# Kernel optimization log

Measured on AMD Instinct MI355X. Metric: run time of the kernel, lower is better.

The kernel has to match this reference:

```python
import jax, jax.numpy as jnp
import numpy as np

H1, H, OUT, T = 512, 2048, 1024, 4096

def setup_inputs() -> dict:
    key = jax.random.key(0)
    ks = jax.random.split(key, 20)
    s = 0.02
    return {
        "input": jax.random.normal(ks[0], (1, OUT), jnp.float32),
        "hidden": jax.random.normal(ks[1], (1, 1, H), jnp.float32) * 0.1,
        "encoder_outputs": jax.random.normal(ks[2], (T, H), jnp.float32),
        "prenet_w": jax.random.normal(ks[3], (H1, OUT), jnp.float32) * s,
        "prenet_b": jnp.zeros((H1,), jnp.float32),
        "prenet2_w": jax.random.normal(ks[4], (H, H1), jnp.float32) * s,
        "prenet2_b": jnp.zeros((H,), jnp.float32),
        "attn1_w": jax.random.normal(ks[5], (H, H), jnp.float32) * s,
        "attn2_w": jax.random.normal(ks[6], (H, H), jnp.float32) * s,
        "attn3_w": jax.random.normal(ks[7], (1, H), jnp.float32) * s,
        "gru_w_ih": jax.random.normal(ks[8], (3 * H, 2 * H), jnp.float32) * s,
        "gru_w_hh": jax.random.normal(ks[9], (3 * H, H), jnp.float32) * s,
        "gru_b_ih": jnp.zeros((3 * H,), jnp.float32),
        "gru_b_hh": jnp.zeros((3 * H,), jnp.float32),
        "lin_w": jax.random.normal(ks[10], (OUT, H), jnp.float32) * s,
        "lin_b": jnp.zeros((OUT,), jnp.float32),
    }

def reference(input, hidden, encoder_outputs, prenet_w, prenet_b, prenet2_w,
              prenet2_b, attn1_w, attn2_w, attn3_w, gru_w_ih, gru_w_hh,
              gru_b_ih, gru_b_hh, lin_w, lin_b):
    # prenet MLP (dropout in eval mode = identity)
    em6 = jax.nn.relu(jax.nn.relu(input @ prenet_w.T + prenet_b) @ prenet2_w.T + prenet2_b)  # [1,H]
    # Bahdanau additive attention
    way = em6 @ attn1_w.T                                 # [1,H]
    uah = encoder_outputs @ attn2_w.T                     # [T,H]
    beta = jnp.tanh(way + uah)                            # [T,H] (broadcast = expand_as)
    gamma = beta @ attn3_w.T                              # [T,1]
    attn_weights = jax.nn.softmax(gamma.T, axis=1)        # [1,T]
    attn_applied = attn_weights @ encoder_outputs         # [1,H]
    # single-step GRU (PyTorch gate order: r, z, n)
    x = jnp.concatenate([em6, attn_applied], axis=1)      # [1,2H]
    h0 = hidden[0]                                        # [1,H]
    gi = x @ gru_w_ih.T + gru_b_ih                        # [1,3H]
    gh = h0 @ gru_w_hh.T + gru_b_hh                       # [1,3H]
    i_r, i_z, i_n = jnp.split(gi, 3, axis=1)
    h_r, h_z, h_n = jnp.split(gh, 3, axis=1)
    r = jax.nn.sigmoid(i_r + h_r)
    z = jax.nn.sigmoid(i_z + h_z)
    n = jnp.tanh(i_n + r * h_n)
    h_new = (1.0 - z) * n + z * h0                        # [1,H]
    out = jax.nn.softmax(h_new @ lin_w.T + lin_b, axis=1) # [1,OUT]
    return out, h_new[None], attn_weights
```

## Files before the change

kernel.cpp:

```cpp
#include <hip/hip_runtime.h>
#include <hip/hip_bf16.h>

typedef __bf16 bf16x8 __attribute__((ext_vector_type(8)));
typedef __bf16 bf16x4 __attribute__((ext_vector_type(4)));
typedef float f32x4 __attribute__((ext_vector_type(4)));

#define H1 512
#define H 2048
#define OUTN 1024
#define T 4096

__global__ __launch_bounds__(256) void matvec_k(
    const float* __restrict__ W, const float* __restrict__ x,
    const float* __restrict__ b, float* __restrict__ out,
    int R, int K, int relu)
{
    int row = blockIdx.x * 4 + (threadIdx.x >> 6);
    int lane = threadIdx.x & 63;
    if (row >= R) return;
    const float* Wr = W + (size_t)row * K;
    float s = 0.f;
    for (int k = lane * 4; k < K; k += 256) {
        float4 w4 = *(const float4*)(Wr + k);
        float4 x4 = *(const float4*)(x + k);
        s += w4.x * x4.x + w4.y * x4.y + w4.z * x4.z + w4.w * x4.w;
    }
    #pragma unroll
    for (int m = 32; m; m >>= 1) s += __shfl_xor(s, m, 64);
    if (lane == 0) {
        if (b) s += b[row];
        if (relu) s = fmaxf(s, 0.f);
        out[row] = s;
    }
}

__global__ __launch_bounds__(256) void cvt_frag_k(
    const float* __restrict__ E, const float* __restrict__ W2,
    __bf16* __restrict__ dst)
{
    const int EC = T * H / 8;
    int c = blockIdx.x * 256 + threadIdx.x;
    const float* src;
    __bf16* d;
    if (c < EC) {
        int lane = c & 63;
        int k32 = (c >> 6) & 63;
        int r16 = c >> 12;
        int row = r16 * 16 + (lane & 15);
        int col = k32 * 32 + (lane >> 4) * 8;
        src = E + (size_t)row * H + col;
        d = dst + (size_t)c * 8;
    } else {
        int c2 = c - EC;
        int row = c2 >> 8;
        int kc = c2 & 255;
        src = W2 + (size_t)row * H + kc * 8;
        int grp = kc >> 3, cc = kc & 7;
        int sw = cc ^ (row & 7);
        d = dst + (size_t)T * H + (size_t)row * H + grp * 64 + sw * 8;
    }
    float4 a = *(const float4*)src;
    float4 b = *(const float4*)(src + 4);
    bf16x8 v = {(__bf16)a.x, (__bf16)a.y, (__bf16)a.z, (__bf16)a.w,
                (__bf16)b.x, (__bf16)b.y, (__bf16)b.z, (__bf16)b.w};
    *(bf16x8*)d = v;
}

__global__ __launch_bounds__(256, 4) void gamma_gemm8(
    const __bf16* __restrict__ Efrag,
    const __bf16* __restrict__ Bsw,
    const float* __restrict__ way, const float* __restrict__ a3,
    float* __restrict__ gamma)
{
    __shared__ __attribute__((aligned(16))) __bf16 Bs[64][64];
    __shared__ float wayS[64], a3S[64];

    const int tb = blockIdx.x, hb = blockIdx.y;
    const int tid = threadIdx.x, lane = tid & 63, wid = tid >> 6;
    if (tid < 64) { wayS[tid] = way[hb * 64 + tid]; a3S[tid] = a3[hb * 64 + tid]; }

    const int K = 2048;
    const int rl = lane & 15;
    const int kg = (lane >> 4) * 8;
    const __bf16* Abase = Efrag + (((size_t)(tb * 8 + wid * 2) * 64) * 64 + lane) * 8;
    const __bf16* Bp = Bsw + (size_t)(hb * 64) * K;

    f32x4 acc[2][4] = {};

    for (int t = 0; t < 32; ++t) {
        const int k0 = t * 64;
        #pragma unroll
        for (int j = 0; j < 2; ++j) {
            int c = tid + j * 256;
            int row_ = c >> 3, cc_ = c & 7;
            const __bf16* s_ = Bp + (size_t)row_ * K + k0 + cc_ * 8;
            __builtin_amdgcn_global_load_lds(
                (const __attribute__((address_space(1))) void*)s_,
                (__attribute__((address_space(3))) void*)((char*)&Bs[0][0] + c * 16),
                16, 0, 0);
        }
        bf16x8 af[2][2];
        #pragma unroll
        for (int mi = 0; mi < 2; ++mi)
            #pragma unroll
            for (int kk = 0; kk < 2; ++kk)
                af[mi][kk] = *(const bf16x8*)(Abase +
                    ((size_t)(mi * 64 + t * 2 + kk) * 64) * 8);

        __syncthreads();

        #pragma unroll
        for (int kk = 0; kk < 2; ++kk) {
            bf16x8 bfm[4];
            const int kb = (kg + kk * 32) * 2;
            #pragma unroll
            for (int ni = 0; ni < 4; ++ni) {
                int r_ = ni * 16 + rl;
                bfm[ni] = *(const bf16x8*)((const char*)&Bs[0][0] + r_ * 128 + (kb ^ ((r_ & 7) << 4)));
            }
            #pragma unroll
            for (int mi = 0; mi < 2; ++mi)
                #pragma unroll
                for (int ni = 0; ni < 4; ++ni)
                    acc[mi][ni] = __builtin_amdgcn_mfma_f32_16x16x32_bf16(
                        af[mi][kk], bfm[ni], acc[mi][ni], 0, 0, 0);
        }
        __syncthreads();
    }

    const int rg = lane >> 4;
    #pragma unroll
    for (int mi = 0; mi < 2; ++mi) {
        float sr[4] = {0.f, 0.f, 0.f, 0.f};
        #pragma unroll
        for (int ni = 0; ni < 4; ++ni) {
            int h = ni * 16 + rl;
            float wh = wayS[h];
            float ah = a3S[h];
            #pragma unroll
            for (int r = 0; r < 4; ++r)
                sr[r] += tanhf(wh + acc[mi][ni][r]) * ah;
        }
        #pragma unroll
        for (int m = 1; m < 16; m <<= 1) {
            #pragma unroll
            for (int r = 0; r < 4; ++r)
                sr[r] += __shfl_xor(sr[r], m, 64);
        }
        if (rl == 0) {
            int t = tb * 128 + wid * 32 + mi * 16 + rg * 4;
            #pragma unroll
            for (int r = 0; r < 4; ++r)
                atomicAdd(&gamma[t + r], sr[r]);
        }
    }
}

#define BM 128
#define BN 128
#define BK 32
#define LSTR 40

__global__ __launch_bounds__(256) void gamma_gemm(
    const float* __restrict__ E, const float* __restrict__ W2,
    const float* __restrict__ way, const float* __restrict__ a3,
    float* __restrict__ gamma)
{
    __shared__ __bf16 As[BM][LSTR];
    __shared__ __bf16 Bs[BN][LSTR];
    __shared__ float wayS[BN];
    __shared__ float a3S[BN];

    const int tb = blockIdx.x, hb = blockIdx.y;
    const int tid = threadIdx.x, lane = tid & 63, wid = tid >> 6;
    const int wr = wid >> 1, wc = wid & 1;
    if (tid < BN) { wayS[tid] = way[hb * BN + tid]; a3S[tid] = a3[hb * BN + tid]; }

    f32x4 acc[4][4] = {};
    const int K = 2048;
    const float* Ep  = E  + (size_t)(tb * BM) * K;
    const float* W2p = W2 + (size_t)(hb * BN) * K;
    const int rl = lane & 15;
    const int kg = (lane >> 4) * 8;

    for (int k0 = 0; k0 < K; k0 += BK) {
        __syncthreads();
        #pragma unroll
        for (int i = 0; i < 4; ++i) {
            int c = tid + i * 256;
            int row = c >> 3;
            int col = (c & 7) * 4;
            float4 va = *(const float4*)(Ep + (size_t)row * K + k0 + col);
            bf16x4 pa = {(__bf16)va.x, (__bf16)va.y, (__bf16)va.z, (__bf16)va.w};
            *(bf16x4*)&As[row][col] = pa;
            float4 vb = *(const float4*)(W2p + (size_t)row * K + k0 + col);
            bf16x4 pb = {(__bf16)vb.x, (__bf16)vb.y, (__bf16)vb.z, (__bf16)vb.w};
            *(bf16x4*)&Bs[row][col] = pb;
        }
        __syncthreads();
        bf16x8 af[4], bfr[4];
        #pragma unroll
        for (int mi = 0; mi < 4; ++mi)
            af[mi] = *(const bf16x8*)&As[wr * 64 + mi * 16 + rl][kg];
        #pragma unroll
        for (int ni = 0; ni < 4; ++ni)
            bfr[ni] = *(const bf16x8*)&Bs[wc * 64 + ni * 16 + rl][kg];
        #pragma unroll
        for (int mi = 0; mi < 4; ++mi)
            #pragma unroll
            for (int ni = 0; ni < 4; ++ni)
                acc[mi][ni] = __builtin_amdgcn_mfma_f32_16x16x32_bf16(
                    af[mi], bfr[ni], acc[mi][ni], 0, 0, 0);
    }

    const int rg = lane >> 4;
    #pragma unroll
    for (int mi = 0; mi < 4; ++mi) {
        float sr[4] = {0.f, 0.f, 0.f, 0.f};
        #pragma unroll
        for (int ni = 0; ni < 4; ++ni) {
            int h = wc * 64 + ni * 16 + rl;
            float wh = wayS[h];
            float ah = a3S[h];
            #pragma unroll
            for (int r = 0; r < 4; ++r)
                sr[r] += tanhf(wh + acc[mi][ni][r]) * ah;
        }
        #pragma unroll
        for (int m = 1; m < 16; m <<= 1) {
            #pragma unroll
            for (int r = 0; r < 4; ++r)
                sr[r] += __shfl_xor(sr[r], m, 64);
        }
        if (rl == 0) {
            int t = tb * BM + wr * 64 + mi * 16 + rg * 4;
            #pragma unroll
            for (int r = 0; r < 4; ++r)
                atomicAdd(&gamma[t + r], sr[r]);
        }
    }
}

__global__ __launch_bounds__(1024) void softmax_k(
    const float* __restrict__ in, float* __restrict__ out, int n)
{
    __shared__ float sred[16];
    __shared__ float sbc;
    int tid = threadIdx.x;

    float m = -3.4e38f;
    for (int i = tid; i < n; i += 1024) m = fmaxf(m, in[i]);
    #pragma unroll
    for (int s = 32; s; s >>= 1) m = fmaxf(m, __shfl_xor(m, s, 64));
    if ((tid & 63) == 0) sred[tid >> 6] = m;
    __syncthreads();
    if (tid == 0) {
        float mm = sred[0];
        for (int i = 1; i < 16; ++i) mm = fmaxf(mm, sred[i]);
        sbc = mm;
    }
    __syncthreads();
    float mx = sbc;

    float s = 0.f;
    for (int i = tid; i < n; i += 1024) s += expf(in[i] - mx);
    #pragma unroll
    for (int sh = 32; sh; sh >>= 1) s += __shfl_xor(s, sh, 64);
    if ((tid & 63) == 0) sred[tid >> 6] = s;
    __syncthreads();
    if (tid == 0) {
        float ss = 0.f;
        for (int i = 0; i < 16; ++i) ss += sred[i];
        sbc = ss;
    }
    __syncthreads();
    float inv = 1.f / sbc;
    for (int i = tid; i < n; i += 1024) out[i] = expf(in[i] - mx) * inv;
}

__global__ __launch_bounds__(256) void attn_apply_k(
    const float* __restrict__ E, const float* __restrict__ w,
    float* __restrict__ outacc)
{
    int tid = threadIdx.x;
    int t0 = blockIdx.x * 32;
    float a[8] = {0.f, 0.f, 0.f, 0.f, 0.f, 0.f, 0.f, 0.f};
    for (int t = t0; t < t0 + 32; ++t) {
        float wt = w[t];
        const float* Er = E + (size_t)t * H;
        #pragma unroll
        for (int j = 0; j < 8; ++j)
            a[j] += wt * Er[tid + 256 * j];
    }
    #pragma unroll
    for (int j = 0; j < 8; ++j)
        atomicAdd(&outacc[tid + 256 * j], a[j]);
}

__global__ __launch_bounds__(256) void gru_combine_k(
    const float* __restrict__ gi, const float* __restrict__ gh,
    const float* __restrict__ h0, float* __restrict__ hout)
{
    int h = blockIdx.x * 256 + threadIdx.x;
    float ir = gi[h], iz = gi[H + h], in_ = gi[2 * H + h];
    float hr = gh[h], hz = gh[H + h], hn = gh[2 * H + h];
    float r = 1.f / (1.f + expf(-(ir + hr)));
    float z = 1.f / (1.f + expf(-(iz + hz)));
    float n = tanhf(in_ + r * hn);
    hout[h] = (1.f - z) * n + z * h0[h];
}

extern "C" void kernel_launch(void* const* d_in, const int* in_sizes, int n_in,
                              void* d_out, int out_size, void* d_ws, size_t ws_size,
                              hipStream_t stream)
{
    const float* input    = (const float*)d_in[0];
    const float* hidden   = (const float*)d_in[1];
    const float* enc      = (const float*)d_in[2];
    const float* prenet_w = (const float*)d_in[3];
    const float* prenet_b = (const float*)d_in[4];
    const float* prenet2_w= (const float*)d_in[5];
    const float* prenet2_b= (const float*)d_in[6];
    const float* attn1_w  = (const float*)d_in[7];
    const float* attn2_w  = (const float*)d_in[8];
    const float* attn3_w  = (const float*)d_in[9];
    const float* gru_w_ih = (const float*)d_in[10];
    const float* gru_w_hh = (const float*)d_in[11];
    const float* gru_b_ih = (const float*)d_in[12];
    const float* gru_b_hh = (const float*)d_in[13];
    const float* lin_w    = (const float*)d_in[14];
    const float* lin_b    = (const float*)d_in[15];

    float* out = (float*)d_out;
    float* h_new = out + OUTN;
    float* attn_w = out + OUTN + H;

    float* ws = (float*)d_ws;
    float* w_h1     = ws;
    float* w_way    = w_h1 + 512;
    float* w_gamma  = w_way + H;
    float* w_x      = w_gamma + T;
    float* w_gi     = w_x + 2 * H;
    float* w_gh     = w_gi + 3 * H;
    float* w_logits = w_gh + 3 * H;

    const size_t BF_OFF = 131072;
    const size_t BF_BYTES = (size_t)(T + H) * H * sizeof(__bf16);
    bool fast = (ws_size >= BF_OFF + BF_BYTES);
    __bf16* bfE  = (__bf16*)((char*)d_ws + BF_OFF);
    __bf16* bfW2 = bfE + (size_t)T * H;

    hipMemsetAsync(w_gamma, 0, T * sizeof(float), stream);
    hipMemsetAsync(w_x + H, 0, H * sizeof(float), stream);

    if (fast)
        cvt_frag_k<<<(T + H) * (H / 8) / 256, 256, 0, stream>>>(enc, attn2_w, bfE);

    matvec_k<<<H1 / 4, 256, 0, stream>>>(prenet_w, input, prenet_b, w_h1, H1, OUTN, 1);
    matvec_k<<<H / 4, 256, 0, stream>>>(prenet2_w, w_h1, prenet2_b, w_x, H, H1, 1);
    matvec_k<<<H / 4, 256, 0, stream>>>(attn1_w, w_x, nullptr, w_way, H, H, 0);

    if (fast)
        gamma_gemm8<<<dim3(T / 128, H / 64), 256, 0, stream>>>(bfE, bfW2, w_way, attn3_w, w_gamma);
    else
        gamma_gemm<<<dim3(T / BM, H / BN), 256, 0, stream>>>(enc, attn2_w, w_way, attn3_w, w_gamma);

    softmax_k<<<1, 1024, 0, stream>>>(w_gamma, attn_w, T);
    attn_apply_k<<<T / 32, 256, 0, stream>>>(enc, attn_w, w_x + H);
    matvec_k<<<(3 * H) / 4, 256, 0, stream>>>(gru_w_ih, w_x, gru_b_ih, w_gi, 3 * H, 2 * H, 0);
    matvec_k<<<(3 * H) / 4, 256, 0, stream>>>(gru_w_hh, hidden, gru_b_hh, w_gh, 3 * H, H, 0);
    gru_combine_k<<<H / 256, 256, 0, stream>>>(w_gi, w_gh, hidden, h_new);
    matvec_k<<<OUTN / 4, 256, 0, stream>>>(lin_w, h_new, lin_b, w_logits, OUTN, H, 0);
    softmax_k<<<1, 1024, 0, stream>>>(w_logits, out, OUTN);
}
```

Measured before the change: 127.6 us.

## Double gamma GEMM K-tile, replace atomics with partials, fuse GRU matvecs

The gamma GEMM now loads 128-wide K tiles per iteration, halving the number of barrier-synchronised steps. Each hb-block writes its partial gamma sums to a separate buffer instead of using atomicAdd, and a new single-block softmax reduces the 32 partials before normalising, which also removes the gamma memset. The two GRU matvecs and the combine kernel are fused into one kernel that computes all three gates per hidden unit. The cost is double the LDS use per GEMM block and a single-block softmax that reads 32x more data.

```diff
diff --git a/kernel.cpp b/kernel.cpp
--- a/kernel.cpp
+++ b/kernel.cpp
@@ -66,13 +66,13 @@
     *(bf16x8*)d = v;
 }
 
-__global__ __launch_bounds__(256, 4) void gamma_gemm8(
+__global__ __launch_bounds__(256, 4) void gamma_gemm9(
     const __bf16* __restrict__ Efrag,
     const __bf16* __restrict__ Bsw,
     const float* __restrict__ way, const float* __restrict__ a3,
-    float* __restrict__ gamma)
-{
-    __shared__ __attribute__((aligned(16))) __bf16 Bs[64][64];
+    float* __restrict__ gpart)
+{
+    __shared__ __attribute__((aligned(16))) __bf16 Bs[64][128];
     __shared__ float wayS[64], a3S[64];
 
     const int tb = blockIdx.x, hb = blockIdx.y;
@@ -87,36 +87,36 @@
 
     f32x4 acc[2][4] = {};
 
-    for (int t = 0; t < 32; ++t) {
-        const int k0 = t * 64;
-        #pragma unroll
-        for (int j = 0; j < 2; ++j) {
+    for (int t = 0; t < 16; ++t) {
+        const int k0 = t * 128;
+        #pragma unroll
+        for (int j = 0; j < 4; ++j) {
             int c = tid + j * 256;
-            int row_ = c >> 3, cc_ = c & 7;
-            const __bf16* s_ = Bp + (size_t)row_ * K + k0 + cc_ * 8;
+            int row_ = c >> 4, grp_ = (c >> 3) & 1, cc_ = c & 7;
+            const __bf16* s_ = Bp + (size_t)row_ * K + k0 + grp_ * 64 + cc_ * 8;
             __builtin_amdgcn_global_load_lds(
                 (const __attribute__((address_space(1))) void*)s_,
                 (__attribute__((address_space(3))) void*)((char*)&Bs[0][0] + c * 16),
                 16, 0, 0);
         }
-        bf16x8 af[2][2];
+        bf16x8 af[2][4];
         #pragma unroll
         for (int mi = 0; mi < 2; ++mi)
             #pragma unroll
-            for (int kk = 0; kk < 2; ++kk)
+            for (int kk = 0; kk < 4; ++kk)
                 af[mi][kk] = *(const bf16x8*)(Abase +
-                    ((size_t)(mi * 64 + t * 2 + kk) * 64) * 8);
+                    ((size_t)(mi * 64 + t * 4 + kk) * 64) * 8);
 
         __syncthreads();
 
         #pragma unroll
-        for (int kk = 0; kk < 2; ++kk) {
+        for (int kk = 0; kk < 4; ++kk) {
             bf16x8 bfm[4];
-            const int kb = (kg + kk * 32) * 2;
+            const int kb = kg * 2 + kk * 64;
             #pragma unroll
             for (int ni = 0; ni < 4; ++ni) {
                 int r_ = ni * 16 + rl;
-                bfm[ni] = *(const bf16x8*)((const char*)&Bs[0][0] + r_ * 128 + (kb ^ ((r_ & 7) << 4)));
+                bfm[ni] = *(const bf16x8*)((const char*)&Bs[0][0] + r_ * 256 + (kb ^ ((r_ & 7) << 4)));
             }
             #pragma unroll
             for (int mi = 0; mi < 2; ++mi)
@@ -148,11 +148,110 @@
                 sr[r] += __shfl_xor(sr[r], m, 64);
         }
         if (rl == 0) {
-            int t = tb * 128 + wid * 32 + mi * 16 + rg * 4;
-            #pragma unroll
-            for (int r = 0; r < 4; ++r)
-                atomicAdd(&gamma[t + r], sr[r]);
-        }
+            int t_ = tb * 128 + wid * 32 + mi * 16 + rg * 4;
+            #pragma unroll
+            for (int r = 0; r < 4; ++r)
+                gpart[hb * T + t_ + r] = sr[r];
+        }
+    }
+}
+
+__global__ __launch_bounds__(1024) void softmax_gamma_k(
+    const float* __restrict__ gpart, float* __restrict__ outw)
+{
+    __shared__ float sred[16];
+    __shared__ float sbcM, sbcS;
+    int tid = threadIdx.x;
+    float g[4];
+    float m = -3.4e38f;
+    #pragma unroll
+    for (int p = 0; p < 4; ++p) {
+        int t = tid + p * 1024;
+        float s = 0.f;
+        for (int hb = 0; hb < 32; ++hb) s += gpart[hb * T + t];
+        g[p] = s;
+        m = fmaxf(m, s);
+    }
+    #pragma unroll
+    for (int sh = 32; sh; sh >>= 1) m = fmaxf(m, __shfl_xor(m, sh, 64));
+    if ((tid & 63) == 0) sred[tid >> 6] = m;
+    __syncthreads();
+    if (tid == 0) {
+        float mm = sred[0];
+        for (int i = 1; i < 16; ++i) mm = fmaxf(mm, sred[i]);
+        sbcM = mm;
+    }
+    __syncthreads();
+    float mx = sbcM;
+    float ssum = 0.f;
+    #pragma unroll
+    for (int p = 0; p < 4; ++p) { g[p] = expf(g[p] - mx); ssum += g[p]; }
+    #pragma unroll
+    for (int sh = 32; sh; sh >>= 1) ssum += __shfl_xor(ssum, sh, 64);
+    __syncthreads();
+    if ((tid & 63) == 0) sred[tid >> 6] = ssum;
+    __syncthreads();
+    if (tid == 0) {
+        float ss = 0.f;
+        for (int i = 0; i < 16; ++i) ss += sred[i];
+        sbcS = ss;
+    }
+    __syncthreads();
+    float inv = 1.f / sbcS;
+    #pragma unroll
+    for (int p = 0; p < 4; ++p) outw[tid + p * 1024] = g[p] * inv;
+}
+
+__global__ __launch_bounds__(256) void gru_fused_k(
+    const float* __restrict__ w_ih,
+    const float* __restrict__ w_hh,
+    const float* __restrict__ b_ih, const float* __restrict__ b_hh,
+    const float* __restrict__ x,
+    const float* __restrict__ h0,
+    float* __restrict__ hout)
+{
+    int h = blockIdx.x * 4 + (threadIdx.x >> 6);
+    int lane = threadIdx.x & 63;
+    const float* wiR = w_ih + (size_t)h * (2 * H);
+    const float* wiZ = w_ih + (size_t)(H + h) * (2 * H);
+    const float* wiN = w_ih + (size_t)(2 * H + h) * (2 * H);
+    const float* whR = w_hh + (size_t)h * H;
+    const float* whZ = w_hh + (size_t)(H + h) * H;
+    const float* whN = w_hh + (size_t)(2 * H + h) * H;
+
+    float sR = 0.f, sZ = 0.f, sN = 0.f, sHN = 0.f;
+    for (int k = lane * 4; k < 2 * H; k += 256) {
+        float4 xv = *(const float4*)(x + k);
+        float4 a = *(const float4*)(wiR + k);
+        sR += a.x * xv.x + a.y * xv.y + a.z * xv.z + a.w * xv.w;
+        float4 b = *(const float4*)(wiZ + k);
+        sZ += b.x * xv.x + b.y * xv.y + b.z * xv.z + b.w * xv.w;
+        float4 c = *(const float4*)(wiN + k);
+        sN += c.x * xv.x + c.y * xv.y + c.z * xv.z + c.w * xv.w;
+    }
+    for (int k = lane * 4; k < H; k += 256) {
+        float4 hv = *(const float4*)(h0 + k);
+        float4 a = *(const float4*)(whR + k);
+        sR += a.x * hv.x + a.y * hv.y + a.z * hv.z + a.w * hv.w;
+        float4 b = *(const float4*)(whZ + k);
+        sZ += b.x * hv.x + b.y * hv.y + b.z * hv.z + b.w * hv.w;
+        float4 c = *(const float4*)(whN + k);
+        sHN += c.x * hv.x + c.y * hv.y + c.z * hv.z + c.w * hv.w;
+    }
+    #pragma unroll
+    for (int m = 32; m; m >>= 1) {
+        sR += __shfl_xor(sR, m, 64);
+        sZ += __shfl_xor(sZ, m, 64);
+        sN += __shfl_xor(sN, m, 64);
+        sHN += __shfl_xor(sHN, m, 64);
+    }
+    if (lane == 0) {
+        float r = 1.f / (1.f + expf(-(sR + b_ih[h] + b_hh[h])));
+        float z = 1.f / (1.f + expf(-(sZ + b_ih[H + h] + b_hh[H + h])));
+        float iN = sN + b_ih[2 * H + h];
+        float hN = sHN + b_hh[2 * H + h];
+        float n = tanhf(iN + r * hN);
+        hout[h] = (1.f - z) * n + z * h0[h];
     }
 }
 
@@ -295,19 +394,6 @@
     #pragma unroll
     for (int j = 0; j < 8; ++j)
         atomicAdd(&outacc[tid + 256 * j], a[j]);
-}
-
-__global__ __launch_bounds__(256) void gru_combine_k(
-    const float* __restrict__ gi, const float* __restrict__ gh,
-    const float* __restrict__ h0, float* __restrict__ hout)
-{
-    int h = blockIdx.x * 256 + threadIdx.x;
-    float ir = gi[h], iz = gi[H + h], in_ = gi[2 * H + h];
-    float hr = gh[h], hz = gh[H + h], hn = gh[2 * H + h];
-    float r = 1.f / (1.f + expf(-(ir + hr)));
-    float z = 1.f / (1.f + expf(-(iz + hz)));
-    float n = tanhf(in_ + r * hn);
-    hout[h] = (1.f - z) * n + z * h0[h];
 }
 
 extern "C" void kernel_launch(void* const* d_in, const int* in_sizes, int n_in,
@@ -338,19 +424,16 @@
     float* ws = (float*)d_ws;
     float* w_h1     = ws;
     float* w_way    = w_h1 + 512;
-    float* w_gamma  = w_way + H;
-    float* w_x      = w_gamma + T;
-    float* w_gi     = w_x + 2 * H;
-    float* w_gh     = w_gi + 3 * H;
-    float* w_logits = w_gh + 3 * H;
-
-    const size_t BF_OFF = 131072;
+    float* w_x      = w_way + H;
+    float* w_logits = w_x + 2 * H;
+    float* w_gpart  = w_logits + OUTN;
+
+    const size_t BF_OFF = 1 << 20;
     const size_t BF_BYTES = (size_t)(T + H) * H * sizeof(__bf16);
     bool fast = (ws_size >= BF_OFF + BF_BYTES);
     __bf16* bfE  = (__bf16*)((char*)d_ws + BF_OFF);
     __bf16* bfW2 = bfE + (size_t)T * H;
 
-    hipMemsetAsync(w_gamma, 0, T * sizeof(float), stream);
     hipMemsetAsync(w_x + H, 0, H * sizeof(float), stream);
 
     if (fast)
@@ -360,16 +443,18 @@
     matvec_k<<<H / 4, 256, 0, stream>>>(prenet2_w, w_h1, prenet2_b, w_x, H, H1, 1);
     matvec_k<<<H / 4, 256, 0, stream>>>(attn1_w, w_x, nullptr, w_way, H, H, 0);
 
-    if (fast)
-        gamma_gemm8<<<dim3(T / 128, H / 64), 256, 0, stream>>>(bfE, bfW2, w_way, attn3_w, w_gamma);
-    else
-        gamma_gemm<<<dim3(T / BM, H / BN), 256, 0, stream>>>(enc, attn2_w, w_way, attn3_w, w_gamma);
-
-    softmax_k<<<1, 1024, 0, stream>>>(w_gamma, attn_w, T);
+    if (fast) {
+        gamma_gemm9<<<dim3(T / 128, H / 64), 256, 0, stream>>>(bfE, bfW2, w_way, attn3_w, w_gpart);
+        softmax_gamma_k<<<1, 1024, 0, stream>>>(w_gpart, attn_w);
+    } else {
+        hipMemsetAsync(w_gpart, 0, T * sizeof(float), stream);
+        gamma_gemm<<<dim3(T / BM, H / BN), 256, 0, stream>>>(enc, attn2_w, w_way, attn3_w, w_gpart);
+        softmax_k<<<1, 1024, 0, stream>>>(w_gpart, attn_w, T);
+    }
+
     attn_apply_k<<<T / 32, 256, 0, stream>>>(enc, attn_w, w_x + H);
-    matvec_k<<<(3 * H) / 4, 256, 0, stream>>>(gru_w_ih, w_x, gru_b_ih, w_gi, 3 * H, 2 * H, 0);
-    matvec_k<<<(3 * H) / 4, 256, 0, stream>>>(gru_w_hh, hidden, gru_b_hh, w_gh, 3 * H, H, 0);
-    gru_combine_k<<<H / 256, 256, 0, stream>>>(w_gi, w_gh, hidden, h_new);
+    gru_fused_k<<<H / 4, 256, 0, stream>>>(gru_w_ih, gru_w_hh, gru_b_ih, gru_b_hh,
+                                           w_x, hidden, h_new);
     matvec_k<<<OUTN / 4, 256, 0, stream>>>(lin_w, h_new, lin_b, w_logits, OUTN, H, 0);
     softmax_k<<<1, 1024, 0, stream>>>(w_logits, out, OUTN);
 }
```

Result: slower. 157.9 us (+23.7%).
